# Kernel optimization log

Hardware: AMD Instinct MI355X
Metric: run time of the kernel (lower is better)

Reference implementation:

```python
import jax, jax.numpy as jnp
import numpy as np

N_NODES = 100000
N_EDGES = 600000
IN_DIM = 128
HID = 128
N_GRAPHS = 512
N_CLASSES = 10


def setup_inputs() -> dict:
    key = jax.random.key(0)
    ks = jax.random.split(key, 8)
    feats = jax.random.normal(ks[0], (N_NODES, IN_DIM), dtype=jnp.float32)
    W = jax.random.normal(ks[1], (IN_DIM, HID), dtype=jnp.float32) * 0.05
    b = jnp.zeros((HID,), dtype=jnp.float32)
    W1 = jax.random.normal(ks[2], (HID, 12), dtype=jnp.float32) * 0.05
    b1 = jnp.zeros((12,), dtype=jnp.float32)
    W2 = jax.random.normal(ks[3], (12, N_CLASSES), dtype=jnp.float32) * 0.05
    b2 = jnp.zeros((N_CLASSES,), dtype=jnp.float32)
    src = jax.random.randint(ks[4], (N_EDGES,), 0, N_NODES, dtype=jnp.int32)
    dst = jax.random.randint(ks[5], (N_EDGES,), 0, N_NODES, dtype=jnp.int32)
    graph_ids = jnp.sort(jax.random.randint(ks[6], (N_NODES,), 0, N_GRAPHS, dtype=jnp.int32))
    return {"feats": feats, "W": W, "b": b, "W1": W1, "b1": b1, "W2": W2,
            "b2": b2, "src": src, "dst": dst, "graph_ids": graph_ids}


def reference(feats, W, b, W1, b1, W2, b2, src, dst, graph_ids):
    ones_e = jnp.ones((src.shape[0],), dtype=feats.dtype)
    # DGL GraphConv norm='both': clamp degrees to >= 1
    out_deg = jnp.maximum(jax.ops.segment_sum(ones_e, src, num_segments=N_NODES), 1.0)
    in_deg = jnp.maximum(jax.ops.segment_sum(ones_e, dst, num_segments=N_NODES), 1.0)
    norm_src = out_deg ** -0.5  # [N]
    norm_dst = in_deg ** -0.5
    x = feats * norm_src[:, None]               # scale source features
    agg = jax.ops.segment_sum(x[src], dst, num_segments=N_NODES)  # gather-scatter SpMM
    h = agg * norm_dst[:, None]
    h = jnp.maximum(h @ W + b, 0.0)             # GraphConv linear + ReLU  [N, HID]
    # mean_nodes: per-graph segment mean (empty graphs -> 0, matching DGL)
    gsum = jax.ops.segment_sum(h, graph_ids, num_segments=N_GRAPHS)
    cnt = jax.ops.segment_sum(jnp.ones((N_NODES,), h.dtype), graph_ids, num_segments=N_GRAPHS)
    hg = jnp.where(cnt[:, None] > 0, gsum / jnp.maximum(cnt, 1.0)[:, None], 0.0)
    # tiny 2-layer MLP classifier
    return (hg @ W1 + b1) @ W2 + b2             # [N_GRAPHS, N_CLASSES]
```

## Files before the change

kernel.cpp:

```cpp
#include <hip/hip_runtime.h>
#include <hip/hip_fp16.h>

#define N_NODES 100000
#define N_EDGES 600000
#define DIM 128
#define N_GRAPHS 512
#define MLP_HID 12
#define N_CLASSES 10
#define NPB 16
#define SLOT_CAP 32
#define TPAD 136
#define YPAD 132
#define EPT 4
#define NBLK (N_NODES / NPB)

#define EDGE_BLOCKS ((N_EDGES + 256*EPT - 1) / (256*EPT))
#define GEMM_BLOCKS (NBLK / 2)
#define INIT_ZERO_BLOCKS ((2 * N_NODES + 255) / 256)

typedef _Float16 half8 __attribute__((ext_vector_type(8)));
typedef float float4v __attribute__((ext_vector_type(4)));
typedef float floatx2 __attribute__((ext_vector_type(2)));

__global__ void init_kernel(const float* __restrict__ W, __half* __restrict__ wfrag,
                            int* __restrict__ hists ) {
    int bx = blockIdx.x;
    if (bx < 8) {
        int item = bx * 256 + threadIdx.x;
        int lane = item & 63;
        int kt = (item >> 6) & 3;
        int nt = item >> 8;
        int n = nt * 16 + (lane & 15);
        int k0 = kt * 32 + (lane >> 4) * 8;
        union { int4 i4; __half h[8]; } u;
        #pragma unroll
        for (int j = 0; j < 8; ++j) u.h[j] = __float2half(W[(k0 + j) * DIM + n]);
        ((int4*)wfrag)[item] = u.i4;
        return;
    }
    int i = (bx - 8) * 256 + threadIdx.x;
    if (i < 2 * N_NODES) hists[i] = 0;
}

__global__ void prep_kernel(const int* __restrict__ src, const int* __restrict__ dst,
                            int* __restrict__ out_hist, int* __restrict__ in_hist,
                            int* __restrict__ slots,
                            const __half* __restrict__ wfrag,
                            const float4* __restrict__ feats4, int* __restrict__ yq) {
    int bx = blockIdx.x;
    if (bx < EDGE_BLOCKS) {
        int base = bx * (256 * EPT) + threadIdx.x;
        int s[EPT], d[EPT]; bool ok[EPT];
        #pragma unroll
        for (int e = 0; e < EPT; ++e) {
            int i = base + e * 256;
            ok[e] = (i < N_EDGES);
            s[e] = ok[e] ? src[i] : 0;
            d[e] = ok[e] ? dst[i] : 0;
        }
        #pragma unroll
        for (int e = 0; e < EPT; ++e) if (ok[e]) atomicAdd(&out_hist[s[e]], 1);
        int tk[EPT];
        #pragma unroll
        for (int e = 0; e < EPT; ++e) tk[e] = ok[e] ? atomicAdd(&in_hist[d[e]], 1) : SLOT_CAP;
        #pragma unroll
        for (int e = 0; e < EPT; ++e)
            if (tk[e] < SLOT_CAP) slots[d[e] * SLOT_CAP + tk[e]] = s[e];
        return;
    }
    __shared__ __half tile_h[2][NPB][TPAD];
    __shared__ float ytile[2][NPB][YPAD];
    int tid = threadIdx.x;
    int u = tid >> 7;
    int t = tid & 127;
    int tile = (bx - EDGE_BLOCKS) * 2 + u;
    int node0 = tile * NPB;

    #pragma unroll
    for (int it = 0; it < 4; ++it) {
        int f = it * 128 + t;
        int node = f >> 5;
        int k4 = f & 31;
        float4 v = feats4[(size_t)(node0 + node) * 32 + k4];
        union { int2 q; __half2 h[2]; } st;
        st.h[0] = __floats2half2_rn(v.x, v.y);
        st.h[1] = __floats2half2_rn(v.z, v.w);
        *(int2*)&tile_h[u][node][k4 * 4] = st.q;
    }
    __syncthreads();

    int wave = t >> 6;
    int wl = t & 63;
    int quad = wl >> 4;
    int col = wl & 15;

    half8 afrag[4];
    #pragma unroll
    for (int kt = 0; kt < 4; ++kt)
        afrag[kt] = *reinterpret_cast<const half8*>(&tile_h[u][col][kt * 32 + quad * 8]);

    float4v c[4];
    #pragma unroll
    for (int nt = 0; nt < 4; ++nt) { c[nt][0] = 0.f; c[nt][1] = 0.f; c[nt][2] = 0.f; c[nt][3] = 0.f; }

    #pragma unroll
    for (int nt = 0; nt < 4; ++nt) {
        int ntile = wave * 4 + nt;
        #pragma unroll
        for (int kt = 0; kt < 4; ++kt) {
            half8 bfrag = *reinterpret_cast<const half8*>(wfrag + ((size_t)(ntile * 4 + kt) * 64 + wl) * 8);
            c[nt] = __builtin_amdgcn_mfma_f32_16x16x32_f16(afrag[kt], bfrag, c[nt], 0, 0, 0);
        }
    }

    #pragma unroll
    for (int nt = 0; nt < 4; ++nt) {
        #pragma unroll
        for (int i2 = 0; i2 < 4; ++i2)
            ytile[u][quad * 4 + i2][(wave * 4 + nt) * 16 + col] = c[nt][i2];
    }
    __syncthreads();

    {
        int node = t >> 3;
        int kg = t & 7;
        const float* yr = &ytile[u][node][kg * 16];
        float4 y0 = *(const float4*)(yr + 0);
        float4 y1 = *(const float4*)(yr + 4);
        float4 y2 = *(const float4*)(yr + 8);
        float4 y3 = *(const float4*)(yr + 12);
        int d0 = __builtin_amdgcn_cvt_pk_fp8_f32(y0.x, y0.y, 0, false);
        d0     = __builtin_amdgcn_cvt_pk_fp8_f32(y0.z, y0.w, d0, true);
        int d1 = __builtin_amdgcn_cvt_pk_fp8_f32(y1.x, y1.y, 0, false);
        d1     = __builtin_amdgcn_cvt_pk_fp8_f32(y1.z, y1.w, d1, true);
        int d2 = __builtin_amdgcn_cvt_pk_fp8_f32(y2.x, y2.y, 0, false);
        d2     = __builtin_amdgcn_cvt_pk_fp8_f32(y2.z, y2.w, d2, true);
        int d3 = __builtin_amdgcn_cvt_pk_fp8_f32(y3.x, y3.y, 0, false);
        d3     = __builtin_amdgcn_cvt_pk_fp8_f32(y3.z, y3.w, d3, true);
        *(int4*)&yq[(size_t)(node0 + node) * 32 + kg * 4] = make_int4(d0, d1, d2, d3);
    }
}

__global__ __launch_bounds__(128) void gather_kernel(
        const int* __restrict__ yq,
        const int* __restrict__ in_hist, const int* __restrict__ out_hist,
        const int* __restrict__ slots,
        const float* __restrict__ bvec, const int* __restrict__ gid,
        float* __restrict__ partial, __half* __restrict__ mixed_h) {
    __shared__ float pl[2][DIM];
    int t = threadIdx.x;
    int group = t >> 5;
    int lane = t & 31;
    int node0 = blockIdx.x * NPB;

    int dv = 0;
    if (lane < 16) dv = in_hist[node0 + lane];
    int deg[4]; int es[4]; float nsf[4];
    #pragma unroll
    for (int r = 0; r < 4; ++r) {
        int j = r * 4 + group;
        deg[r] = __shfl(dv, j, 32);
        int m = min(deg[r], SLOT_CAP);
        es[r] = 0;
        if (lane < m) es[r] = slots[(node0 + j) * SLOT_CAP + lane];
        nsf[r] = 0.f;
        if (lane < m) nsf[r] = rsqrtf((float)max(out_hist[es[r]], 1));
    }

    float4 bb = *(const float4*)&bvec[lane * 4];
    bool uni = (gid[node0] == gid[node0 + NPB - 1]);
    float4 pool = make_float4(0.f, 0.f, 0.f, 0.f);

    #pragma unroll
    for (int r = 0; r < 4; ++r) {
        int j = r * 4 + group;
        int m = min(deg[r], SLOT_CAP);
        float4 a4 = make_float4(0.f, 0.f, 0.f, 0.f);
        int i = 0;
        for (; i + 4 <= m; i += 4) {
            int sn0 = __shfl(es[r], i + 0, 32), sn1 = __shfl(es[r], i + 1, 32);
            int sn2 = __shfl(es[r], i + 2, 32), sn3 = __shfl(es[r], i + 3, 32);
            float ns0 = __shfl(nsf[r], i + 0, 32), ns1 = __shfl(nsf[r], i + 1, 32);
            float ns2 = __shfl(nsf[r], i + 2, 32), ns3 = __shfl(nsf[r], i + 3, 32);
            int q0 = yq[sn0 * 32 + lane];
            int q1 = yq[sn1 * 32 + lane];
            int q2 = yq[sn2 * 32 + lane];
            int q3 = yq[sn3 * 32 + lane];
            floatx2 p0 = __builtin_amdgcn_cvt_pk_f32_fp8(q0, false);
            floatx2 r0 = __builtin_amdgcn_cvt_pk_f32_fp8(q0, true);
            floatx2 p1 = __builtin_amdgcn_cvt_pk_f32_fp8(q1, false);
            floatx2 r1 = __builtin_amdgcn_cvt_pk_f32_fp8(q1, true);
            floatx2 p2 = __builtin_amdgcn_cvt_pk_f32_fp8(q2, false);
            floatx2 r2 = __builtin_amdgcn_cvt_pk_f32_fp8(q2, true);
            floatx2 p3 = __builtin_amdgcn_cvt_pk_f32_fp8(q3, false);
            floatx2 r3 = __builtin_amdgcn_cvt_pk_f32_fp8(q3, true);
            a4.x = fmaf(p0[0], ns0, fmaf(p1[0], ns1, fmaf(p2[0], ns2, fmaf(p3[0], ns3, a4.x))));
            a4.y = fmaf(p0[1], ns0, fmaf(p1[1], ns1, fmaf(p2[1], ns2, fmaf(p3[1], ns3, a4.y))));
            a4.z = fmaf(r0[0], ns0, fmaf(r1[0], ns1, fmaf(r2[0], ns2, fmaf(r3[0], ns3, a4.z))));
            a4.w = fmaf(r0[1], ns0, fmaf(r1[1], ns1, fmaf(r2[1], ns2, fmaf(r3[1], ns3, a4.w))));
        }
        for (; i < m; ++i) {
            int sn = __shfl(es[r], i, 32);
            float nsv = __shfl(nsf[r], i, 32);
            int q = yq[sn * 32 + lane];
            floatx2 p = __builtin_amdgcn_cvt_pk_f32_fp8(q, false);
            floatx2 rr = __builtin_amdgcn_cvt_pk_f32_fp8(q, true);
            a4.x = fmaf(p[0], nsv, a4.x);
            a4.y = fmaf(p[1], nsv, a4.y);
            a4.z = fmaf(rr[0], nsv, a4.z);
            a4.w = fmaf(rr[1], nsv, a4.w);
        }
        float nd = rsqrtf((float)max(deg[r], 1));
        float4 h;
        h.x = fmaxf(fmaf(a4.x, nd, bb.x), 0.f);
        h.y = fmaxf(fmaf(a4.y, nd, bb.y), 0.f);
        h.z = fmaxf(fmaf(a4.z, nd, bb.z), 0.f);
        h.w = fmaxf(fmaf(a4.w, nd, bb.w), 0.f);
        if (uni) {
            pool.x += h.x; pool.y += h.y; pool.z += h.z; pool.w += h.w;
        } else {
            union { int2 v; __half2 h2[2]; } st;
            st.h2[0] = __floats2half2_rn(h.x, h.y);
            st.h2[1] = __floats2half2_rn(h.z, h.w);
            *(int2*)&mixed_h[(size_t)blockIdx.x * (NPB * DIM) + j * DIM + lane * 4] = st.v;
        }
    }

    if (uni) {
        pool.x += __shfl_xor(pool.x, 32, 64);
        pool.y += __shfl_xor(pool.y, 32, 64);
        pool.z += __shfl_xor(pool.z, 32, 64);
        pool.w += __shfl_xor(pool.w, 32, 64);
        int wave = t >> 6, wl = t & 63;
        if (wl < 32) *(float4*)&pl[wave][wl * 4] = pool;
        __syncthreads();
        if (t < DIM) partial[blockIdx.x * DIM + t] = pl[0][t] + pl[1][t];
    }
}

__device__ __forceinline__ int lower_bound_i(const int* __restrict__ a, int n, int v) {
    int lo = 0, hi = n;
    while (lo < hi) { int mid = (lo + hi) >> 1; if (a[mid] < v) lo = mid + 1; else hi = mid; }
    return lo;
}

__global__ __launch_bounds__(128) void mlp_kernel(
        const float* __restrict__ partial, const __half* __restrict__ mixed_h,
        const int* __restrict__ gid,
        const float* __restrict__ W1, const float* __restrict__ b1,
        const float* __restrict__ W2, const float* __restrict__ b2,
        float* __restrict__ out) {
    __shared__ float s[DIM];
    __shared__ float t1[MLP_HID];
    int g = blockIdx.x;
    int t = threadIdx.x;
    int s_g = lower_bound_i(gid, N_NODES, g);
    int e_g = lower_bound_i(gid, N_NODES, g + 1);
    float cntf = (float)(e_g - s_g);
    float acc = 0.f;
    int b_lo = (s_g + NPB - 1) >> 4;
    int b_hi = e_g >> 4;
    if (b_lo < b_hi) {
        for (int b = b_lo; b < b_hi; ++b) acc += partial[b * DIM + t];
        for (int n = s_g; n < b_lo * NPB; ++n)
            acc += __half2float(mixed_h[(size_t)(n >> 4) * (NPB * DIM) + (n & 15) * DIM + t]);
        for (int n = b_hi * NPB; n < e_g; ++n)
            acc += __half2float(mixed_h[(size_t)(n >> 4) * (NPB * DIM) + (n & 15) * DIM + t]);
    } else {
        for (int n = s_g; n < e_g; ++n)
            acc += __half2float(mixed_h[(size_t)(n >> 4) * (NPB * DIM) + (n & 15) * DIM + t]);
    }
    s[t] = (cntf > 0.f) ? (acc / cntf) : 0.f;
    __syncthreads();
    if (t < MLP_HID) {
        float a = b1[t];
        for (int k = 0; k < DIM; ++k) a = fmaf(s[k], W1[k * MLP_HID + t], a);
        t1[t] = a;
    }
    __syncthreads();
    if (t < N_CLASSES) {
        float o = b2[t];
        #pragma unroll
        for (int j = 0; j < MLP_HID; ++j) o = fmaf(t1[j], W2[j * N_CLASSES + t], o);
        out[g * N_CLASSES + t] = o;
    }
}

extern "C" void kernel_launch(void* const* d_in, const int* in_sizes, int n_in,
                              void* d_out, int out_size, void* d_ws, size_t ws_size,
                              hipStream_t stream) {
    const float* feats = (const float*)d_in[0];
    const float* W     = (const float*)d_in[1];
    const float* b     = (const float*)d_in[2];
    const float* W1    = (const float*)d_in[3];
    const float* b1    = (const float*)d_in[4];
    const float* W2    = (const float*)d_in[5];
    const float* b2    = (const float*)d_in[6];
    const int*   src   = (const int*)d_in[7];
    const int*   dst   = (const int*)d_in[8];
    const int*   gid   = (const int*)d_in[9];
    float* out = (float*)d_out;

    char* ws = (char*)d_ws;
    int*   out_hist = (int*)ws;   ws += (size_t)N_NODES * 4;
    int*   in_hist  = (int*)ws;   ws += (size_t)N_NODES * 4;
    ws = (char*)(((uintptr_t)ws + 255) & ~(uintptr_t)255);
    int*    slots   = (int*)ws;    ws += (size_t)N_NODES * SLOT_CAP * 4;
    int*    yq      = (int*)ws;    ws += (size_t)N_NODES * DIM;
    __half* wfrag   = (__half*)ws; ws += (size_t)2048 * 8 * 2;
    ws = (char*)(((uintptr_t)ws + 255) & ~(uintptr_t)255);
    float*  partial = (float*)ws;  ws += (size_t)NBLK * DIM * 4;
    __half* mixed_h = (__half*)ws; ws += (size_t)NBLK * NPB * DIM * 2;

    init_kernel<<<8 + INIT_ZERO_BLOCKS, 256, 0, stream>>>(W, wfrag, out_hist);

    prep_kernel<<<EDGE_BLOCKS + GEMM_BLOCKS, 256, 0, stream>>>(
        src, dst, out_hist, in_hist, slots, wfrag, (const float4*)feats, yq);

    gather_kernel<<<NBLK, 128, 0, stream>>>(
        yq, in_hist, out_hist, slots, b, gid, partial, mixed_h);

    mlp_kernel<<<N_GRAPHS, 128, 0, stream>>>(partial, mixed_h, gid, W1, b1, W2, b2, out);
}
```

Measured before the change: 200.3 us.

## Privatize degree histograms and slot lists per XCD with XCD-scoped atomics

```diff
diff --git a/kernel.cpp b/kernel.cpp
--- a/kernel.cpp
+++ b/kernel.cpp
@@ -8,22 +8,43 @@
 #define MLP_HID 12
 #define N_CLASSES 10
 #define NPB 16
-#define SLOT_CAP 32
+#define NXCD 8
+#define CAPX 16
 #define TPAD 136
 #define YPAD 132
-#define EPT 4
+#define EPT 2
 #define NBLK (N_NODES / NPB)
 
 #define EDGE_BLOCKS ((N_EDGES + 256*EPT - 1) / (256*EPT))
 #define GEMM_BLOCKS (NBLK / 2)
-#define INIT_ZERO_BLOCKS ((2 * N_NODES + 255) / 256)
+#define HIST_INTS (2 * NXCD * N_NODES)
+#define INIT_ZERO_BLOCKS ((HIST_INTS / 4 + 255) / 256)
+#define REDUCE_BLOCKS ((N_NODES + 255) / 256)
 
 typedef _Float16 half8 __attribute__((ext_vector_type(8)));
 typedef float float4v __attribute__((ext_vector_type(4)));
 typedef float floatx2 __attribute__((ext_vector_type(2)));
 
+__device__ __forceinline__ int xcc_id() {
+    unsigned x;
+    asm volatile("s_getreg_b32 %0, hwreg(20, 0, 4)" : "=s"(x));
+    return (int)(x & (NXCD - 1));
+}
+
+__device__ __forceinline__ int atomic_add_xcd_ret(int* p, int v) {
+    int old;
+    asm volatile("global_atomic_add %0, %1, %2, off sc0\n\t"
+                 "s_waitcnt vmcnt(0)"
+                 : "=v"(old) : "v"(p), "v"(v) : "memory");
+    return old;
+}
+__device__ __forceinline__ void atomic_inc_xcd(int* p) {
+    int one = 1;
+    asm volatile("global_atomic_add %0, %1, off" :: "v"(p), "v"(one) : "memory");
+}
+
 __global__ void init_kernel(const float* __restrict__ W, __half* __restrict__ wfrag,
-                            int* __restrict__ hists ) {
+                            int4* __restrict__ hists4) {
     int bx = blockIdx.x;
     if (bx < 8) {
         int item = bx * 256 + threadIdx.x;
@@ -39,37 +60,33 @@
         return;
     }
     int i = (bx - 8) * 256 + threadIdx.x;
-    if (i < 2 * N_NODES) hists[i] = 0;
+    if (i < HIST_INTS / 4) hists4[i] = make_int4(0, 0, 0, 0);
 }
 
 __global__ void prep_kernel(const int* __restrict__ src, const int* __restrict__ dst,
-                            int* __restrict__ out_hist, int* __restrict__ in_hist,
+                            int* __restrict__ out_hist_x, int* __restrict__ in_hist_x,
                             int* __restrict__ slots,
                             const __half* __restrict__ wfrag,
                             const float4* __restrict__ feats4, int* __restrict__ yq) {
+    __shared__ __half tile_h[2][NPB][TPAD];
+    __shared__ float ytile[2][NPB][YPAD];
     int bx = blockIdx.x;
     if (bx < EDGE_BLOCKS) {
+        int xcc = xcc_id();
         int base = bx * (256 * EPT) + threadIdx.x;
-        int s[EPT], d[EPT]; bool ok[EPT];
         #pragma unroll
         for (int e = 0; e < EPT; ++e) {
             int i = base + e * 256;
-            ok[e] = (i < N_EDGES);
-            s[e] = ok[e] ? src[i] : 0;
-            d[e] = ok[e] ? dst[i] : 0;
-        }
-        #pragma unroll
-        for (int e = 0; e < EPT; ++e) if (ok[e]) atomicAdd(&out_hist[s[e]], 1);
-        int tk[EPT];
-        #pragma unroll
-        for (int e = 0; e < EPT; ++e) tk[e] = ok[e] ? atomicAdd(&in_hist[d[e]], 1) : SLOT_CAP;
-        #pragma unroll
-        for (int e = 0; e < EPT; ++e)
-            if (tk[e] < SLOT_CAP) slots[d[e] * SLOT_CAP + tk[e]] = s[e];
+            if (i < N_EDGES) {
+                int s = src[i];
+                int d = dst[i];
+                atomic_inc_xcd(&out_hist_x[xcc * N_NODES + s]);
+                int tk = atomic_add_xcd_ret(&in_hist_x[xcc * N_NODES + d], 1);
+                if (tk < CAPX) slots[((size_t)d * NXCD + xcc) * CAPX + tk] = s;
+            }
+        }
         return;
     }
-    __shared__ __half tile_h[2][NPB][TPAD];
-    __shared__ float ytile[2][NPB][YPAD];
     int tid = threadIdx.x;
     int u = tid >> 7;
     int t = tid & 127;
@@ -141,10 +158,21 @@
     }
 }
 
+__global__ __launch_bounds__(256) void reduce_kernel(const int* __restrict__ out_hist_x,
+                                                     float* __restrict__ ninv) {
+    int n = blockIdx.x * 256 + threadIdx.x;
+    if (n < N_NODES) {
+        int s = 0;
+        #pragma unroll
+        for (int x = 0; x < NXCD; ++x) s += out_hist_x[x * N_NODES + n];
+        ninv[n] = rsqrtf((float)max(s, 1));
+    }
+}
+
 __global__ __launch_bounds__(128) void gather_kernel(
         const int* __restrict__ yq,
-        const int* __restrict__ in_hist, const int* __restrict__ out_hist,
-        const int* __restrict__ slots,
+        const int* __restrict__ in_hist_x, const int* __restrict__ slots,
+        const float* __restrict__ ninv,
         const float* __restrict__ bvec, const int* __restrict__ gid,
         float* __restrict__ partial, __half* __restrict__ mixed_h) {
     __shared__ float pl[2][DIM];
@@ -153,18 +181,39 @@
     int lane = t & 31;
     int node0 = blockIdx.x * NPB;
 
-    int dv = 0;
-    if (lane < 16) dv = in_hist[node0 + lane];
-    int deg[4]; int es[4]; float nsf[4];
+    int degt[4]; int ms[4]; int es[4]; float nsf[4];
     #pragma unroll
     for (int r = 0; r < 4; ++r) {
         int j = r * 4 + group;
-        deg[r] = __shfl(dv, j, 32);
-        int m = min(deg[r], SLOT_CAP);
-        es[r] = 0;
-        if (lane < m) es[r] = slots[(node0 + j) * SLOT_CAP + lane];
-        nsf[r] = 0.f;
-        if (lane < m) nsf[r] = rsqrtf((float)max(out_hist[es[r]], 1));
+        int node = node0 + j;
+        int ctrue = 0;
+        if (lane < 8) ctrue = in_hist_x[lane * N_NODES + node];
+        int c = min(ctrue, CAPX);
+        int dt = ctrue;
+        dt += __shfl_xor(dt, 1, 8);
+        dt += __shfl_xor(dt, 2, 8);
+        dt += __shfl_xor(dt, 4, 8);
+        degt[r] = __shfl(dt, 0, 32);
+        int ic = c;
+        int u1 = __shfl_up(ic, 1, 8); if ((lane & 7) >= 1) ic += u1;
+        int u2 = __shfl_up(ic, 2, 8); if ((lane & 7) >= 2) ic += u2;
+        int u3 = __shfl_up(ic, 4, 8); if ((lane & 7) >= 4) ic += u3;
+        int ex = ic - c;
+        int totc = __shfl(ic, 7, 32);
+        ms[r] = min(totc, 32);
+        int pk = (ex << 16) | c;
+        int sx = 0, sidx = 0;
+        #pragma unroll
+        for (int x = 0; x < 8; ++x) {
+            int p = __shfl(pk, x, 32);
+            int ebx = p >> 16, ecx = p & 0xffff;
+            if (lane >= ebx && lane < ebx + ecx) { sx = x; sidx = lane - ebx; }
+        }
+        es[r] = 0; nsf[r] = 0.f;
+        if (lane < ms[r]) {
+            es[r] = slots[((size_t)node * NXCD + sx) * CAPX + sidx];
+            nsf[r] = ninv[es[r]];
+        }
     }
 
     float4 bb = *(const float4*)&bvec[lane * 4];
@@ -174,7 +223,7 @@
     #pragma unroll
     for (int r = 0; r < 4; ++r) {
         int j = r * 4 + group;
-        int m = min(deg[r], SLOT_CAP);
+        int m = ms[r];
         float4 a4 = make_float4(0.f, 0.f, 0.f, 0.f);
         int i = 0;
         for (; i + 4 <= m; i += 4) {
@@ -210,7 +259,7 @@
             a4.z = fmaf(rr[0], nsv, a4.z);
             a4.w = fmaf(rr[1], nsv, a4.w);
         }
-        float nd = rsqrtf((float)max(deg[r], 1));
+        float nd = rsqrtf((float)max(degt[r], 1));
         float4 h;
         h.x = fmaxf(fmaf(a4.x, nd, bb.x), 0.f);
         h.y = fmaxf(fmaf(a4.y, nd, bb.y), 0.f);
@@ -302,23 +351,26 @@
     float* out = (float*)d_out;
 
     char* ws = (char*)d_ws;
-    int*   out_hist = (int*)ws;   ws += (size_t)N_NODES * 4;
-    int*   in_hist  = (int*)ws;   ws += (size_t)N_NODES * 4;
+    int*   out_hist_x = (int*)ws;  ws += (size_t)NXCD * N_NODES * 4;
+    int*   in_hist_x  = (int*)ws;  ws += (size_t)NXCD * N_NODES * 4;
     ws = (char*)(((uintptr_t)ws + 255) & ~(uintptr_t)255);
-    int*    slots   = (int*)ws;    ws += (size_t)N_NODES * SLOT_CAP * 4;
+    int*    slots   = (int*)ws;    ws += (size_t)N_NODES * NXCD * CAPX * 4;
     int*    yq      = (int*)ws;    ws += (size_t)N_NODES * DIM;
+    float*  ninv    = (float*)ws;  ws += (size_t)N_NODES * 4;
     __half* wfrag   = (__half*)ws; ws += (size_t)2048 * 8 * 2;
     ws = (char*)(((uintptr_t)ws + 255) & ~(uintptr_t)255);
     float*  partial = (float*)ws;  ws += (size_t)NBLK * DIM * 4;
     __half* mixed_h = (__half*)ws; ws += (size_t)NBLK * NPB * DIM * 2;
 
-    init_kernel<<<8 + INIT_ZERO_BLOCKS, 256, 0, stream>>>(W, wfrag, out_hist);
+    init_kernel<<<8 + INIT_ZERO_BLOCKS, 256, 0, stream>>>(W, wfrag, (int4*)out_hist_x);
 
     prep_kernel<<<EDGE_BLOCKS + GEMM_BLOCKS, 256, 0, stream>>>(
-        src, dst, out_hist, in_hist, slots, wfrag, (const float4*)feats, yq);
+        src, dst, out_hist_x, in_hist_x, slots, wfrag, (const float4*)feats, yq);
+
+    reduce_kernel<<<REDUCE_BLOCKS, 256, 0, stream>>>(out_hist_x, ninv);
 
     gather_kernel<<<NBLK, 128, 0, stream>>>(
-        yq, in_hist, out_hist, slots, b, gid, partial, mixed_h);
+        yq, in_hist_x, slots, ninv, b, gid, partial, mixed_h);
 
     mlp_kernel<<<N_GRAPHS, 128, 0, stream>>>(partial, mixed_h, gid, W1, b1, W2, b2, out);
 }
```

Result: slower. 219.7 us (+9.7%).

## Replace global atomic degree histograms with LDS-partitioned counting and fold source norm into GEMM

Applied to the files above, without the earlier changes.

```diff
diff --git a/kernel.cpp b/kernel.cpp
--- a/kernel.cpp
+++ b/kernel.cpp
@@ -11,19 +11,24 @@
 #define SLOT_CAP 32
 #define TPAD 136
 #define YPAD 132
-#define EPT 4
 #define NBLK (N_NODES / NPB)
 
-#define EDGE_BLOCKS ((N_EDGES + 256*EPT - 1) / (256*EPT))
+#define K_CH 8
+#define R_RG 16
+#define RN (N_NODES / R_RG)
+#define EC (N_EDGES / K_CH)
+#define COUNT_BLOCKS (2 * K_CH * R_RG)
+#define SCATTER_BLOCKS (K_CH * R_RG)
 #define GEMM_BLOCKS (NBLK / 2)
-#define INIT_ZERO_BLOCKS ((2 * N_NODES + 255) / 256)
+#define REDUCE_BLOCKS ((N_NODES + 255) / 256)
 
 typedef _Float16 half8 __attribute__((ext_vector_type(8)));
 typedef float float4v __attribute__((ext_vector_type(4)));
 typedef float floatx2 __attribute__((ext_vector_type(2)));
 
-__global__ void init_kernel(const float* __restrict__ W, __half* __restrict__ wfrag,
-                            int* __restrict__ hists ) {
+__global__ void count_kernel(const int* __restrict__ src, const int* __restrict__ dst,
+                             int* __restrict__ cnt_in_part, int* __restrict__ cnt_out_part,
+                             const float* __restrict__ W, __half* __restrict__ wfrag) {
     int bx = blockIdx.x;
     if (bx < 8) {
         int item = bx * 256 + threadIdx.x;
@@ -38,42 +43,89 @@
         ((int4*)wfrag)[item] = u.i4;
         return;
     }
-    int i = (bx - 8) * 256 + threadIdx.x;
-    if (i < 2 * N_NODES) hists[i] = 0;
-}
-
-__global__ void prep_kernel(const int* __restrict__ src, const int* __restrict__ dst,
-                            int* __restrict__ out_hist, int* __restrict__ in_hist,
-                            int* __restrict__ slots,
-                            const __half* __restrict__ wfrag,
-                            const float4* __restrict__ feats4, int* __restrict__ yq) {
+    __shared__ int cnt[RN];
+    int cb = bx - 8;
+    bool isIn = cb < SCATTER_BLOCKS;
+    int c = isIn ? cb : cb - SCATTER_BLOCKS;
+    int k = c >> 4;
+    int r = c & (R_RG - 1);
+    int nbase = r * RN;
+    const int* arr = isIn ? dst : src;
+    for (int i = threadIdx.x; i < RN; i += 256) cnt[i] = 0;
+    __syncthreads();
+    const int4* a4 = (const int4*)(arr + k * EC);
+    for (int i = threadIdx.x; i < EC / 4; i += 256) {
+        int4 v = a4[i];
+        int vv[4] = { v.x, v.y, v.z, v.w };
+        #pragma unroll
+        for (int e = 0; e < 4; ++e) {
+            unsigned off = (unsigned)(vv[e] - nbase);
+            if (off < RN) atomicAdd(&cnt[off], 1);
+        }
+    }
+    __syncthreads();
+    int* outp = (isIn ? cnt_in_part : cnt_out_part) + k * N_NODES + nbase;
+    for (int i = threadIdx.x; i < RN; i += 256) outp[i] = cnt[i];
+}
+
+__global__ __launch_bounds__(256) void reduce_kernel(
+        int* __restrict__ cnt_in_part, const int* __restrict__ cnt_out_part,
+        int* __restrict__ in_hist, float* __restrict__ ninv) {
+    int n = blockIdx.x * 256 + threadIdx.x;
+    if (n >= N_NODES) return;
+    int s = 0, b[K_CH];
+    #pragma unroll
+    for (int k = 0; k < K_CH; ++k) { b[k] = s; s += cnt_in_part[k * N_NODES + n]; }
+    in_hist[n] = s;
+    #pragma unroll
+    for (int k = 0; k < K_CH; ++k) cnt_in_part[k * N_NODES + n] = b[k];
+    int so = 0;
+    #pragma unroll
+    for (int k = 0; k < K_CH; ++k) so += cnt_out_part[k * N_NODES + n];
+    ninv[n] = rsqrtf((float)max(so, 1));
+}
+
+__global__ void scatter_gemm_kernel(
+        const int* __restrict__ src, const int* __restrict__ dst,
+        const int* __restrict__ base_in, int* __restrict__ slots,
+        const float* __restrict__ ninv,
+        const __half* __restrict__ wfrag,
+        const float4* __restrict__ feats4, int* __restrict__ yq) {
+    union SM {
+        int tk[RN];
+        struct { __half tile[2][NPB][TPAD]; float yt[2][NPB][YPAD]; } g;
+    };
+    __shared__ SM sm;
     int bx = blockIdx.x;
-    if (bx < EDGE_BLOCKS) {
-        int base = bx * (256 * EPT) + threadIdx.x;
-        int s[EPT], d[EPT]; bool ok[EPT];
-        #pragma unroll
-        for (int e = 0; e < EPT; ++e) {
-            int i = base + e * 256;
-            ok[e] = (i < N_EDGES);
-            s[e] = ok[e] ? src[i] : 0;
-            d[e] = ok[e] ? dst[i] : 0;
-        }
-        #pragma unroll
-        for (int e = 0; e < EPT; ++e) if (ok[e]) atomicAdd(&out_hist[s[e]], 1);
-        int tk[EPT];
-        #pragma unroll
-        for (int e = 0; e < EPT; ++e) tk[e] = ok[e] ? atomicAdd(&in_hist[d[e]], 1) : SLOT_CAP;
-        #pragma unroll
-        for (int e = 0; e < EPT; ++e)
-            if (tk[e] < SLOT_CAP) slots[d[e] * SLOT_CAP + tk[e]] = s[e];
+    if (bx < SCATTER_BLOCKS) {
+        int k = bx >> 4;
+        int r = bx & (R_RG - 1);
+        int nbase = r * RN;
+        for (int i = threadIdx.x; i < RN; i += 256)
+            sm.tk[i] = base_in[k * N_NODES + nbase + i];
+        __syncthreads();
+        const int4* d4p = (const int4*)(dst + k * EC);
+        const int4* s4p = (const int4*)(src + k * EC);
+        for (int i = threadIdx.x; i < EC / 4; i += 256) {
+            int4 d4 = d4p[i];
+            int4 s4 = s4p[i];
+            int dd[4] = { d4.x, d4.y, d4.z, d4.w };
+            int ss[4] = { s4.x, s4.y, s4.z, s4.w };
+            #pragma unroll
+            for (int e = 0; e < 4; ++e) {
+                unsigned off = (unsigned)(dd[e] - nbase);
+                if (off < RN) {
+                    int pos = atomicAdd(&sm.tk[off], 1);
+                    if (pos < SLOT_CAP) slots[dd[e] * SLOT_CAP + pos] = ss[e];
+                }
+            }
+        }
         return;
     }
-    __shared__ __half tile_h[2][NPB][TPAD];
-    __shared__ float ytile[2][NPB][YPAD];
     int tid = threadIdx.x;
     int u = tid >> 7;
     int t = tid & 127;
-    int tile = (bx - EDGE_BLOCKS) * 2 + u;
+    int tile = (bx - SCATTER_BLOCKS) * 2 + u;
     int node0 = tile * NPB;
 
     #pragma unroll
@@ -85,7 +137,7 @@
         union { int2 q; __half2 h[2]; } st;
         st.h[0] = __floats2half2_rn(v.x, v.y);
         st.h[1] = __floats2half2_rn(v.z, v.w);
-        *(int2*)&tile_h[u][node][k4 * 4] = st.q;
+        *(int2*)&sm.g.tile[u][node][k4 * 4] = st.q;
     }
     __syncthreads();
 
@@ -97,7 +149,7 @@
     half8 afrag[4];
     #pragma unroll
     for (int kt = 0; kt < 4; ++kt)
-        afrag[kt] = *reinterpret_cast<const half8*>(&tile_h[u][col][kt * 32 + quad * 8]);
+        afrag[kt] = *reinterpret_cast<const half8*>(&sm.g.tile[u][col][kt * 32 + quad * 8]);
 
     float4v c[4];
     #pragma unroll
@@ -117,34 +169,34 @@
     for (int nt = 0; nt < 4; ++nt) {
         #pragma unroll
         for (int i2 = 0; i2 < 4; ++i2)
-            ytile[u][quad * 4 + i2][(wave * 4 + nt) * 16 + col] = c[nt][i2];
+            sm.g.yt[u][quad * 4 + i2][(wave * 4 + nt) * 16 + col] = c[nt][i2];
     }
     __syncthreads();
 
     {
         int node = t >> 3;
         int kg = t & 7;
-        const float* yr = &ytile[u][node][kg * 16];
+        float nsv = ninv[node0 + node];
+        const float* yr = &sm.g.yt[u][node][kg * 16];
         float4 y0 = *(const float4*)(yr + 0);
         float4 y1 = *(const float4*)(yr + 4);
         float4 y2 = *(const float4*)(yr + 8);
         float4 y3 = *(const float4*)(yr + 12);
-        int d0 = __builtin_amdgcn_cvt_pk_fp8_f32(y0.x, y0.y, 0, false);
-        d0     = __builtin_amdgcn_cvt_pk_fp8_f32(y0.z, y0.w, d0, true);
-        int d1 = __builtin_amdgcn_cvt_pk_fp8_f32(y1.x, y1.y, 0, false);
-        d1     = __builtin_amdgcn_cvt_pk_fp8_f32(y1.z, y1.w, d1, true);
-        int d2 = __builtin_amdgcn_cvt_pk_fp8_f32(y2.x, y2.y, 0, false);
-        d2     = __builtin_amdgcn_cvt_pk_fp8_f32(y2.z, y2.w, d2, true);
-        int d3 = __builtin_amdgcn_cvt_pk_fp8_f32(y3.x, y3.y, 0, false);
-        d3     = __builtin_amdgcn_cvt_pk_fp8_f32(y3.z, y3.w, d3, true);
+        int d0 = __builtin_amdgcn_cvt_pk_fp8_f32(y0.x * nsv, y0.y * nsv, 0, false);
+        d0     = __builtin_amdgcn_cvt_pk_fp8_f32(y0.z * nsv, y0.w * nsv, d0, true);
+        int d1 = __builtin_amdgcn_cvt_pk_fp8_f32(y1.x * nsv, y1.y * nsv, 0, false);
+        d1     = __builtin_amdgcn_cvt_pk_fp8_f32(y1.z * nsv, y1.w * nsv, d1, true);
+        int d2 = __builtin_amdgcn_cvt_pk_fp8_f32(y2.x * nsv, y2.y * nsv, 0, false);
+        d2     = __builtin_amdgcn_cvt_pk_fp8_f32(y2.z * nsv, y2.w * nsv, d2, true);
+        int d3 = __builtin_amdgcn_cvt_pk_fp8_f32(y3.x * nsv, y3.y * nsv, 0, false);
+        d3     = __builtin_amdgcn_cvt_pk_fp8_f32(y3.z * nsv, y3.w * nsv, d3, true);
         *(int4*)&yq[(size_t)(node0 + node) * 32 + kg * 4] = make_int4(d0, d1, d2, d3);
     }
 }
 
 __global__ __launch_bounds__(128) void gather_kernel(
         const int* __restrict__ yq,
-        const int* __restrict__ in_hist, const int* __restrict__ out_hist,
-        const int* __restrict__ slots,
+        const int* __restrict__ in_hist, const int* __restrict__ slots,
         const float* __restrict__ bvec, const int* __restrict__ gid,
         float* __restrict__ partial, __half* __restrict__ mixed_h) {
     __shared__ float pl[2][DIM];
@@ -155,7 +207,7 @@
 
     int dv = 0;
     if (lane < 16) dv = in_hist[node0 + lane];
-    int deg[4]; int es[4]; float nsf[4];
+    int deg[4]; int es[4];
     #pragma unroll
     for (int r = 0; r < 4; ++r) {
         int j = r * 4 + group;
@@ -163,8 +215,6 @@
         int m = min(deg[r], SLOT_CAP);
         es[r] = 0;
         if (lane < m) es[r] = slots[(node0 + j) * SLOT_CAP + lane];
-        nsf[r] = 0.f;
-        if (lane < m) nsf[r] = rsqrtf((float)max(out_hist[es[r]], 1));
     }
 
     float4 bb = *(const float4*)&bvec[lane * 4];
@@ -180,8 +230,6 @@
         for (; i + 4 <= m; i += 4) {
             int sn0 = __shfl(es[r], i + 0, 32), sn1 = __shfl(es[r], i + 1, 32);
             int sn2 = __shfl(es[r], i + 2, 32), sn3 = __shfl(es[r], i + 3, 32);
-            float ns0 = __shfl(nsf[r], i + 0, 32), ns1 = __shfl(nsf[r], i + 1, 32);
-            float ns2 = __shfl(nsf[r], i + 2, 32), ns3 = __shfl(nsf[r], i + 3, 32);
             int q0 = yq[sn0 * 32 + lane];
             int q1 = yq[sn1 * 32 + lane];
             int q2 = yq[sn2 * 32 + lane];
@@ -194,21 +242,17 @@
             floatx2 r2 = __builtin_amdgcn_cvt_pk_f32_fp8(q2, true);
             floatx2 p3 = __builtin_amdgcn_cvt_pk_f32_fp8(q3, false);
             floatx2 r3 = __builtin_amdgcn_cvt_pk_f32_fp8(q3, true);
-            a4.x = fmaf(p0[0], ns0, fmaf(p1[0], ns1, fmaf(p2[0], ns2, fmaf(p3[0], ns3, a4.x))));
-            a4.y = fmaf(p0[1], ns0, fmaf(p1[1], ns1, fmaf(p2[1], ns2, fmaf(p3[1], ns3, a4.y))));
-            a4.z = fmaf(r0[0], ns0, fmaf(r1[0], ns1, fmaf(r2[0], ns2, fmaf(r3[0], ns3, a4.z))));
-            a4.w = fmaf(r0[1], ns0, fmaf(r1[1], ns1, fmaf(r2[1], ns2, fmaf(r3[1], ns3, a4.w))));
+            a4.x += p0[0] + p1[0] + p2[0] + p3[0];
+            a4.y += p0[1] + p1[1] + p2[1] + p3[1];
+            a4.z += r0[0] + r1[0] + r2[0] + r3[0];
+            a4.w += r0[1] + r1[1] + r2[1] + r3[1];
         }
         for (; i < m; ++i) {
             int sn = __shfl(es[r], i, 32);
-            float nsv = __shfl(nsf[r], i, 32);
             int q = yq[sn * 32 + lane];
             floatx2 p = __builtin_amdgcn_cvt_pk_f32_fp8(q, false);
             floatx2 rr = __builtin_amdgcn_cvt_pk_f32_fp8(q, true);
-            a4.x = fmaf(p[0], nsv, a4.x);
-            a4.y = fmaf(p[1], nsv, a4.y);
-            a4.z = fmaf(rr[0], nsv, a4.z);
-            a4.w = fmaf(rr[1], nsv, a4.w);
+            a4.x += p[0]; a4.y += p[1]; a4.z += rr[0]; a4.w += rr[1];
         }
         float nd = rsqrtf((float)max(deg[r], 1));
         float4 h;
@@ -302,8 +346,10 @@
     float* out = (float*)d_out;
 
     char* ws = (char*)d_ws;
-    int*   out_hist = (int*)ws;   ws += (size_t)N_NODES * 4;
-    int*   in_hist  = (int*)ws;   ws += (size_t)N_NODES * 4;
+    int*    cnt_in  = (int*)ws;    ws += (size_t)K_CH * N_NODES * 4;
+    int*    cnt_out = (int*)ws;    ws += (size_t)K_CH * N_NODES * 4;
+    int*    in_hist = (int*)ws;    ws += (size_t)N_NODES * 4;
+    float*  ninv    = (float*)ws;  ws += (size_t)N_NODES * 4;
     ws = (char*)(((uintptr_t)ws + 255) & ~(uintptr_t)255);
     int*    slots   = (int*)ws;    ws += (size_t)N_NODES * SLOT_CAP * 4;
     int*    yq      = (int*)ws;    ws += (size_t)N_NODES * DIM;
@@ -312,13 +358,17 @@
     float*  partial = (float*)ws;  ws += (size_t)NBLK * DIM * 4;
     __half* mixed_h = (__half*)ws; ws += (size_t)NBLK * NPB * DIM * 2;
 
-    init_kernel<<<8 + INIT_ZERO_BLOCKS, 256, 0, stream>>>(W, wfrag, out_hist);
-
-    prep_kernel<<<EDGE_BLOCKS + GEMM_BLOCKS, 256, 0, stream>>>(
-        src, dst, out_hist, in_hist, slots, wfrag, (const float4*)feats, yq);
+    count_kernel<<<8 + COUNT_BLOCKS, 256, 0, stream>>>(
+        src, dst, cnt_in, cnt_out, W, wfrag);
+
+    reduce_kernel<<<REDUCE_BLOCKS, 256, 0, stream>>>(
+        cnt_in, cnt_out, in_hist, ninv);
+
+    scatter_gemm_kernel<<<SCATTER_BLOCKS + GEMM_BLOCKS, 256, 0, stream>>>(
+        src, dst, cnt_in, slots, ninv, wfrag, (const float4*)feats, yq);
 
     gather_kernel<<<NBLK, 128, 0, stream>>>(
-        yq, in_hist, out_hist, slots, b, gid, partial, mixed_h);
+        yq, in_hist, slots, b, gid, partial, mixed_h);
 
     mlp_kernel<<<N_GRAPHS, 128, 0, stream>>>(partial, mixed_h, gid, W1, b1, W2, b2, out);
 }
```

After: 228.7 us. 14.2% more time.
